# Performance work log

Hardware: AMD Instinct MI355X
Metric: run time of the kernel (lower is better)

The kernel has to match this reference:

```python
import jax, jax.numpy as jnp
import numpy as np

IN_CH = 512
MID = max(IN_CH // 8, 1)


def setup_inputs() -> dict:
    key = jax.random.key(0)
    ks = jax.random.split(key, 8)
    B, C, H, W = 4, IN_CH, 64, 64
    s = 0.05
    x = jax.random.normal(ks[0], (B, C, H, W), dtype=jnp.float32)
    wq = jax.random.normal(ks[1], (MID, C), dtype=jnp.float32) * s
    bq = jnp.zeros((MID,), dtype=jnp.float32)
    wk = jax.random.normal(ks[2], (MID, C), dtype=jnp.float32) * s
    bk = jnp.zeros((MID,), dtype=jnp.float32)
    wv = jax.random.normal(ks[3], (C, C), dtype=jnp.float32) * s
    bv = jnp.zeros((C,), dtype=jnp.float32)
    alpha = jnp.ones((1,), dtype=jnp.float32) * 0.5  # nonzero so attention path is exercised
    return {"x": x, "wq": wq, "bq": bq, "wk": wk, "bk": bk, "wv": wv, "bv": bv, "alpha": alpha}


def reference(x, wq, bq, wk, bk, wv, bv, alpha):
    B, C, H, W = x.shape
    N = H * W
    xf = x.reshape(B, C, N)  # [B, C, N]
    # 1x1 convs == per-position channel GEMMs
    q = jnp.einsum('mc,bcn->bnm', wq, xf) + bq  # [B, N, mid]
    k = jnp.einsum('mc,bcn->bmn', wk, xf) + bk[None, :, None]  # [B, mid, N]
    v = jnp.einsum('dc,bcn->bdn', wv, xf) + bv[None, :, None]  # [B, C, N]
    attn = jax.nn.softmax(jnp.einsum('bnm,bmk->bnk', q, k), axis=-1)  # [B, N, N]
    out = jnp.einsum('bdn,bkn->bdk', v, attn)  # v @ attn^T -> [B, C, N]
    out = out.reshape(B, C, H, W)
    return alpha * out + x
```

## Files before the change

kernel.cpp:

```cpp
#include <hip/hip_runtime.h>

#define BB 4
#define CD 512
#define NP 4096
#define MID 64

typedef _Float16 half8 __attribute__((ext_vector_type(8)));
typedef _Float16 half4 __attribute__((ext_vector_type(4)));
typedef float floatx4 __attribute__((ext_vector_type(4)));

#define LOG2E 1.4426950408889634f

__global__ __launch_bounds__(256) void prep_w(
    const float* __restrict__ wq, const float* __restrict__ wk,
    const float* __restrict__ wv, const float* __restrict__ bq,
    const float* __restrict__ bk, const float* __restrict__ bv,
    _Float16* __restrict__ w_h, float* __restrict__ bias) {
  int idx = blockIdx.x * 256 + threadIdx.x;
  for (int i = idx; i < 640 * 512; i += gridDim.x * 256) {
    int r = i >> 9, c = i & 511;
    float v = (r < 64) ? wq[(r << 9) + c] * LOG2E
            : (r < 128) ? wk[((r - 64) << 9) + c]
                        : wv[((r - 128) << 9) + c];
    w_h[i] = (_Float16)v;
  }
  if (idx < 640) {
    float v = (idx < 64) ? bq[idx] * LOG2E
            : (idx < 128) ? bk[idx - 64]
                          : bv[idx - 128];
    bias[idx] = v;
  }
}

__global__ __launch_bounds__(256) void transpose_x(const float* __restrict__ x,
                                                   _Float16* __restrict__ xt) {
  __shared__ float tile[64][65];
  int b = blockIdx.z, c0 = blockIdx.y * 64, n0 = blockIdx.x * 64;
  int t = threadIdx.x;
  const float* xb = x + (size_t)b * CD * NP;
#pragma unroll
  for (int k = 0; k < 16; k++) {
    int cl = k * 4 + (t >> 6);
    int nl = t & 63;
    tile[cl][nl] = xb[(size_t)(c0 + cl) * NP + n0 + nl];
  }
  __syncthreads();
  _Float16* xtb = xt + ((size_t)b * NP + n0) * CD + c0;
#pragma unroll
  for (int k = 0; k < 2; k++) {
    int nl = k * 32 + (t >> 3);
    int cl = (t & 7) * 8;
    half8 pk;
#pragma unroll
    for (int i = 0; i < 8; i++) pk[i] = (_Float16)tile[cl + i][nl];
    *(half8*)(xtb + (size_t)nl * CD + cl) = pk;
  }
}

__global__ __launch_bounds__(256, 2) void proj_qkv(
    const _Float16* __restrict__ w_h, const float* __restrict__ bias,
    const _Float16* __restrict__ xt, _Float16* __restrict__ q_h,
    _Float16* __restrict__ k_h, _Float16* __restrict__ v_h) {
  __shared__ _Float16 xls[64 * 512];
  int t = threadIdx.x, w = t >> 6, lane = t & 63;
  int col = lane & 15, quad = lane >> 4;
  int rbh = blockIdx.x, nb = blockIdx.y, b = blockIdx.z;
  int n0 = nb * 64;
  const _Float16* xtb = xt + ((size_t)b * NP + n0) * CD;
#pragma unroll
  for (int j = 0; j < 16; j++) {
    int u = t + j * 256;
    int row = u >> 6, un = u & 63;
    *(half8*)(xls + row * 512 + ((un ^ (row & 7)) << 3)) =
        *(const half8*)(xtb + (size_t)row * CD + un * 8);
  }
  __syncthreads();

  int rw = rbh * 320 + w * 80;
  floatx4 acc[5][4] = {};
  for (int c = 0; c < CD; c += 32) {
    int cu = c >> 3;
    half8 a[5], bf[4];
#pragma unroll
    for (int i = 0; i < 5; i++)
      a[i] = *(const half8*)(w_h + (size_t)(rw + i * 16 + col) * CD + c + quad * 8);
#pragma unroll
    for (int j = 0; j < 4; j++) {
      int row = j * 16 + col;
      bf[j] = *(const half8*)(xls + row * 512 + (((cu + quad) ^ (row & 7)) << 3));
    }
#pragma unroll
    for (int i = 0; i < 5; i++)
#pragma unroll
      for (int j = 0; j < 4; j++)
        acc[i][j] = __builtin_amdgcn_mfma_f32_16x16x32_f16(a[i], bf[j], acc[i][j], 0, 0, 0);
  }

#pragma unroll
  for (int i = 0; i < 5; i++) {
    int r0 = rw + i * 16;
    float bi[4];
#pragma unroll
    for (int rr = 0; rr < 4; rr++) bi[rr] = bias[r0 + quad * 4 + rr];
    if (r0 < 128) {
      _Float16* dst = (r0 < 64 ? q_h + (size_t)b * NP * MID + r0
                               : k_h + (size_t)b * NP * MID + (r0 - 64));
#pragma unroll
      for (int j = 0; j < 4; j++) {
        int n = n0 + j * 16 + col;
        half4 pk;
#pragma unroll
        for (int rr = 0; rr < 4; rr++) pk[rr] = (_Float16)(acc[i][j][rr] + bi[rr]);
        *(half4*)(dst + (size_t)n * MID + quad * 4) = pk;
      }
    } else {
      int dbase = r0 - 128 + quad * 4;
#pragma unroll
      for (int j = 0; j < 4; j++) {
        int n = n0 + j * 16 + col;
#pragma unroll
        for (int rr = 0; rr < 4; rr++)
          v_h[((size_t)b * CD + dbase + rr) * NP + n] =
              (_Float16)(acc[i][j][rr] + bi[rr]);
      }
    }
  }
}

__global__ __launch_bounds__(256) void rowmax(const _Float16* __restrict__ q_h,
                                              const _Float16* __restrict__ k_h,
                                              float* __restrict__ M) {
  int qb = blockIdx.x, b = blockIdx.y;
  int t = threadIdx.x, w = t >> 6, lane = t & 63;
  int col = lane & 15, quad = lane >> 4;
  int q0 = qb * 32;
  const _Float16* qp = q_h + ((size_t)b * NP + q0) * MID;
  half8 bq[2][2];
#pragma unroll
  for (int qt = 0; qt < 2; qt++)
#pragma unroll
    for (int h = 0; h < 2; h++)
      bq[qt][h] = *(const half8*)(qp + (size_t)(qt * 16 + col) * MID + h * 32 + quad * 8);
  const _Float16* kp = k_h + ((size_t)b * NP + (size_t)w * 1024) * MID;
  float m[2] = {-1e30f, -1e30f};
#pragma unroll 4
  for (int n = 0; n < 1024; n += 16) {
    half8 ak0 = *(const half8*)(kp + (size_t)(n + col) * MID + quad * 8);
    half8 ak1 = *(const half8*)(kp + (size_t)(n + col) * MID + 32 + quad * 8);
#pragma unroll
    for (int qt = 0; qt < 2; qt++) {
      floatx4 s = {};
      s = __builtin_amdgcn_mfma_f32_16x16x32_f16(ak0, bq[qt][0], s, 0, 0, 0);
      s = __builtin_amdgcn_mfma_f32_16x16x32_f16(ak1, bq[qt][1], s, 0, 0, 0);
      m[qt] = fmaxf(m[qt], fmaxf(fmaxf(s[0], s[1]), fmaxf(s[2], s[3])));
    }
  }
  __shared__ float red[4][2][16];
#pragma unroll
  for (int qt = 0; qt < 2; qt++) {
    m[qt] = fmaxf(m[qt], __shfl_xor(m[qt], 16));
    m[qt] = fmaxf(m[qt], __shfl_xor(m[qt], 32));
  }
  if (quad == 0) {
    red[w][0][col] = m[0];
    red[w][1][col] = m[1];
  }
  __syncthreads();
  if (t < 32) {
    int qt = t >> 4, c = t & 15;
    float mm = fmaxf(fmaxf(red[0][qt][c], red[1][qt][c]),
                     fmaxf(red[2][qt][c], red[3][qt][c]));
    M[(size_t)b * NP + q0 + t] = mm;
  }
}

#define DMA16(gp, ldsoff)                                                      \
  asm volatile("s_mov_b32 m0, %0\n\t"                                         \
               "global_load_lds_dwordx4 %1, off"                              \
               :: "s"(__builtin_amdgcn_readfirstlane((int)(ldsoff))),          \
                  "v"(gp)                                                      \
               : "memory")

__global__ __launch_bounds__(256, 2) void attn_pv(
    const _Float16* __restrict__ q_h, const _Float16* __restrict__ k_h,
    const _Float16* __restrict__ v_h, const float* __restrict__ M,
    const float* __restrict__ x, const float* __restrict__ alpha_p,
    float* __restrict__ out) {
  int bid = blockIdx.x;
  int combo = bid & 7;
  int b = combo >> 1, ds = combo & 1;
  int qb = bid >> 3;
  int q0 = qb * 64, d0 = ds * 256;

  int t = threadIdx.x, w = t >> 6, lane = t & 63;
  int col = lane & 15, quad = lane >> 4;
  int c7 = col & 7;

  __shared__ floatx4 smem4[50432 / 16];
  char* smem = (char*)smem4;
  char* vbufB = smem;
  char* kbufB = smem + 32768;
  float* lred = (float*)(smem + 49152);
  float* lfin = (float*)(smem + 50176);

  const _Float16* qp = q_h + ((size_t)b * NP + q0) * MID;
  half8 bq[4][2];
#pragma unroll
  for (int qt = 0; qt < 4; qt++)
#pragma unroll
    for (int h = 0; h < 2; h++)
      bq[qt][h] = *(const half8*)(qp + (size_t)(qt * 16 + col) * MID + h * 32 + quad * 8);
  float Mq[4];
#pragma unroll
  for (int qt = 0; qt < 4; qt++) Mq[qt] = M[(size_t)b * NP + q0 + qt * 16 + col];

  int klane = (lane >> 3) * MID + (((lane & 7) ^ ((lane >> 3) & 7)) << 3);
  size_t vlane = (size_t)(lane >> 2) * NP + ((lane & 3) << 3);

  const _Float16* kgb = k_h + (size_t)b * NP * MID;
  const _Float16* vgb = v_h + (size_t)(b * CD + d0 + w * 64) * NP;

  floatx4 acc[4][4] = {};
  float lp[4] = {0.f, 0.f, 0.f, 0.f};

  int kdw = 32768 + w * 2048;
  int vdw = w * 4096;

#pragma unroll
  for (int j = 0; j < 2; j++)
    DMA16(kgb + (size_t)(0 + w * 16 + j * 8) * MID + klane, kdw + j * 1024);
#pragma unroll
  for (int h = 0; h < 2; h++)
#pragma unroll
    for (int j = 0; j < 4; j++)
      DMA16(vgb + (size_t)(j * 16) * NP + h * 32 + vlane,
            h * 16384 + vdw + j * 1024);

  for (int ci = 0; ci < 64; ci++) {
    int p = ci & 1;
    int nxt = ((ci + 1) & 63) * 64;

    asm volatile("s_waitcnt lgkmcnt(0)\n\ts_barrier" ::: "memory");
#pragma unroll
    for (int j = 0; j < 2; j++)
      DMA16(kgb + (size_t)(nxt + w * 16 + j * 8) * MID + klane,
            kdw + (1 - p) * 8192 + j * 1024);

    asm volatile("s_waitcnt vmcnt(10)" ::: "memory");

    const char* kb = kbufB + p * 8192 + w * 2048;
    int sl0 = quad ^ c7;
    half8 ak0 = *(const half8*)(kb + col * 128 + (sl0 << 4));
    half8 ak1 = *(const half8*)(kb + col * 128 + ((sl0 ^ 4) << 4));
    char* pbW = kbufB + p * 8192;
#pragma unroll
    for (int qt = 0; qt < 4; qt++) {
      floatx4 s = {};
      s = __builtin_amdgcn_mfma_f32_16x16x32_f16(ak0, bq[qt][0], s, 0, 0, 0);
      s = __builtin_amdgcn_mfma_f32_16x16x32_f16(ak1, bq[qt][1], s, 0, 0, 0);
      half4 pk;
#pragma unroll
      for (int r = 0; r < 4; r++) {
        float pv = __builtin_amdgcn_exp2f(s[r] - Mq[qt]);
        lp[qt] += pv;
        pk[r] = (_Float16)pv;
      }
      *(half4*)(pbW + w * 2048 + (qt * 16 + col) * 32 + quad * 8) = pk;
    }

    asm volatile("s_waitcnt lgkmcnt(0)\n\ts_barrier" ::: "memory");

#pragma unroll
    for (int h = 0; h < 2; h++) {
      asm volatile("s_waitcnt vmcnt(6)" ::: "memory");
      half8 bp[4];
#pragma unroll
      for (int qt = 0; qt < 4; qt++)
        bp[qt] = *(const half8*)(pbW + (2 * h + (quad >> 1)) * 2048 +
                                 (qt * 16 + col) * 32 + ((quad & 1) << 4));
      const char* vb = vbufB + h * 16384 + vdw;
      half8 av[4];
#pragma unroll
      for (int dt = 0; dt < 4; dt++)
        av[dt] = *(const half8*)(vb + (dt * 16 + col) * 64 + (quad << 4));
      __builtin_amdgcn_s_setprio(1);
#pragma unroll
      for (int dt = 0; dt < 4; dt++)
#pragma unroll
        for (int qt = 0; qt < 4; qt++)
          acc[dt][qt] = __builtin_amdgcn_mfma_f32_16x16x32_f16(av[dt], bp[qt], acc[dt][qt], 0, 0, 0);
      __builtin_amdgcn_s_setprio(0);
#pragma unroll
      for (int j = 0; j < 4; j++)
        DMA16(vgb + (size_t)(j * 16) * NP + nxt + h * 32 + vlane,
              h * 16384 + vdw + j * 1024);
    }
  }

#pragma unroll
  for (int qt = 0; qt < 4; qt++) {
    lp[qt] += __shfl_xor(lp[qt], 16);
    lp[qt] += __shfl_xor(lp[qt], 32);
    if (quad == 0) lred[(w * 4 + qt) * 16 + col] = lp[qt];
  }
  __syncthreads();
  if (t < 64) {
    int qt = t >> 4, c = t & 15;
    float l = lred[(0 + qt) * 16 + c] + lred[(4 + qt) * 16 + c] +
              lred[(8 + qt) * 16 + c] + lred[(12 + qt) * 16 + c];
    lfin[t] = alpha_p[0] / l;
  }
  __syncthreads();

  const float* xp = x + ((size_t)(b * CD + d0) + w * 64) * NP;
  float* op = out + ((size_t)(b * CD + d0) + w * 64) * NP;
#pragma unroll
  for (int dt = 0; dt < 4; dt++)
#pragma unroll
    for (int qt = 0; qt < 4; qt++) {
      float linv = lfin[qt * 16 + col];
#pragma unroll
      for (int r = 0; r < 4; r++) {
        size_t o = (size_t)(dt * 16 + quad * 4 + r) * NP + q0 + qt * 16 + col;
        op[o] = acc[dt][qt][r] * linv + xp[o];
      }
    }
}

extern "C" void kernel_launch(void* const* d_in, const int* in_sizes, int n_in,
                              void* d_out, int out_size, void* d_ws, size_t ws_size,
                              hipStream_t stream) {
  const float* x     = (const float*)d_in[0];
  const float* wq    = (const float*)d_in[1];
  const float* bq    = (const float*)d_in[2];
  const float* wk    = (const float*)d_in[3];
  const float* bk    = (const float*)d_in[4];
  const float* wv    = (const float*)d_in[5];
  const float* bv    = (const float*)d_in[6];
  const float* alpha = (const float*)d_in[7];
  float* out = (float*)d_out;

  char* ws = (char*)d_ws;
  _Float16* w_h  = (_Float16*)(ws);
  float*    bias = (float*)(ws + 655360);
  float*    Mbuf = (float*)(ws + 657920);
  _Float16* xt   = (_Float16*)(ws + 723456);
  _Float16* q_h  = (_Float16*)(ws + 17500672);
  _Float16* k_h  = (_Float16*)(ws + 19597824);
  _Float16* v_h  = (_Float16*)(ws + 21694976);

  prep_w<<<1280, 256, 0, stream>>>(wq, wk, wv, bq, bk, bv, w_h, bias);
  transpose_x<<<dim3(64, 8, BB), 256, 0, stream>>>(x, xt);
  proj_qkv<<<dim3(2, 64, BB), 256, 0, stream>>>(w_h, bias, xt, q_h, k_h, v_h);
  rowmax<<<dim3(128, BB), 256, 0, stream>>>(q_h, k_h, Mbuf);
  attn_pv<<<512, 256, 0, stream>>>(q_h, k_h, v_h, Mbuf, x, alpha, out);
}
```

Baseline: 254.8 us.

## Software-pipeline QK/softmax one chunk ahead of PV with separate P buffer

Restructures the attention main loop so the QK scores and exp for chunk ci are computed while the PV MFMAs consume the P tile from chunk ci-1. P moves into its own double-buffered LDS region, and K becomes single-buffered. This cuts the loop to one barrier per iteration and lets the PV matrix ops overlap the softmax work. It also adds XOR swizzles to the V and P LDS layouts to reduce bank conflicts. In exchange LDS use grows, register pressure rises from holding two halves of operands, and all global loads are drained with vmcnt(0) each iteration.

```diff
diff --git a/kernel.cpp b/kernel.cpp
--- a/kernel.cpp
+++ b/kernel.cpp
@@ -196,12 +196,13 @@
   int col = lane & 15, quad = lane >> 4;
   int c7 = col & 7;
 
-  __shared__ floatx4 smem4[50432 / 16];
+  __shared__ floatx4 smem4[58624 / 16];
   char* smem = (char*)smem4;
   char* vbufB = smem;
   char* kbufB = smem + 32768;
-  float* lred = (float*)(smem + 49152);
-  float* lfin = (float*)(smem + 50176);
+  char* pbufB = smem + 40960;
+  float* lred = (float*)(smem + 57344);
+  float* lfin = (float*)(smem + 58368);
 
   const _Float16* qp = q_h + ((size_t)b * NP + q0) * MID;
   half8 bq[4][2];
@@ -215,7 +216,7 @@
   for (int qt = 0; qt < 4; qt++) Mq[qt] = M[(size_t)b * NP + q0 + qt * 16 + col];
 
   int klane = (lane >> 3) * MID + (((lane & 7) ^ ((lane >> 3) & 7)) << 3);
-  size_t vlane = (size_t)(lane >> 2) * NP + ((lane & 3) << 3);
+  size_t vlane = (size_t)(lane >> 2) * NP + (((lane & 3) ^ ((lane >> 3) & 3)) << 3);
 
   const _Float16* kgb = k_h + (size_t)b * NP * MID;
   const _Float16* vgb = v_h + (size_t)(b * CD + d0 + w * 64) * NP;
@@ -226,9 +227,15 @@
   int kdw = 32768 + w * 2048;
   int vdw = w * 4096;
 
+  int koff0 = col * 128 + ((quad ^ c7) << 4);
+  int koff1 = col * 128 + (((quad ^ c7) ^ 4) << 4);
+  int vswz = (quad ^ ((col >> 1) & 3)) << 4;
+  int pws = ((((quad >> 1) ^ ((col >> 2) & 1)) << 4)) + ((quad & 1) << 3);
+  int prs = (((quad & 1) ^ ((col >> 2) & 1)) << 4);
+
 #pragma unroll
   for (int j = 0; j < 2; j++)
-    DMA16(kgb + (size_t)(0 + w * 16 + j * 8) * MID + klane, kdw + j * 1024);
+    DMA16(kgb + (size_t)(w * 16 + j * 8) * MID + klane, kdw + j * 1024);
 #pragma unroll
   for (int h = 0; h < 2; h++)
 #pragma unroll
@@ -236,23 +243,12 @@
       DMA16(vgb + (size_t)(j * 16) * NP + h * 32 + vlane,
             h * 16384 + vdw + j * 1024);
 
-  for (int ci = 0; ci < 64; ci++) {
-    int p = ci & 1;
-    int nxt = ((ci + 1) & 63) * 64;
-
-    asm volatile("s_waitcnt lgkmcnt(0)\n\ts_barrier" ::: "memory");
-#pragma unroll
-    for (int j = 0; j < 2; j++)
-      DMA16(kgb + (size_t)(nxt + w * 16 + j * 8) * MID + klane,
-            kdw + (1 - p) * 8192 + j * 1024);
-
-    asm volatile("s_waitcnt vmcnt(10)" ::: "memory");
-
-    const char* kb = kbufB + p * 8192 + w * 2048;
-    int sl0 = quad ^ c7;
-    half8 ak0 = *(const half8*)(kb + col * 128 + (sl0 << 4));
-    half8 ak1 = *(const half8*)(kb + col * 128 + ((sl0 ^ 4) << 4));
-    char* pbW = kbufB + p * 8192;
+  asm volatile("s_waitcnt vmcnt(8)" ::: "memory");
+  {
+    const char* kb = kbufB + w * 2048;
+    half8 ak0 = *(const half8*)(kb + koff0);
+    half8 ak1 = *(const half8*)(kb + koff1);
+    char* pbW = pbufB + w * 2048;
 #pragma unroll
     for (int qt = 0; qt < 4; qt++) {
       floatx4 s = {};
@@ -265,36 +261,113 @@
         lp[qt] += pv;
         pk[r] = (_Float16)pv;
       }
-      *(half4*)(pbW + w * 2048 + (qt * 16 + col) * 32 + quad * 8) = pk;
-    }
+      *(half4*)(pbW + (qt * 16 + col) * 32 + pws) = pk;
+    }
+    asm volatile("s_waitcnt lgkmcnt(0)" ::: "memory");
+#pragma unroll
+    for (int j = 0; j < 2; j++)
+      DMA16(kgb + (size_t)(64 + w * 16 + j * 8) * MID + klane, kdw + j * 1024);
+    asm volatile("s_barrier" ::: "memory");
+  }
+
+  for (int ci = 1; ci < 64; ci++) {
+    int p = ci & 1;
+    int nc = ci * 64;
+    int nxt = ((ci + 1) & 63) * 64;
+
+    asm volatile("s_waitcnt vmcnt(0)" ::: "memory");
+
+    const char* kb = kbufB + w * 2048;
+    half8 ak0 = *(const half8*)(kb + koff0);
+    half8 ak1 = *(const half8*)(kb + koff1);
+    const char* pbR = pbufB + (1 - p) * 8192;
+    half8 bp[2][4];
+#pragma unroll
+    for (int h = 0; h < 2; h++)
+#pragma unroll
+      for (int qt = 0; qt < 4; qt++)
+        bp[h][qt] = *(const half8*)(pbR + (2 * h + (quad >> 1)) * 2048 +
+                                    (qt * 16 + col) * 32 + prs);
+    half8 av[2][4];
+#pragma unroll
+    for (int h = 0; h < 2; h++)
+#pragma unroll
+      for (int dt = 0; dt < 4; dt++)
+        av[h][dt] = *(const half8*)(vbufB + h * 16384 + vdw + dt * 1024 +
+                                    col * 64 + vswz);
+
+    floatx4 s[4];
+#pragma unroll
+    for (int qt = 0; qt < 4; qt++) {
+      floatx4 z = {};
+      z = __builtin_amdgcn_mfma_f32_16x16x32_f16(ak0, bq[qt][0], z, 0, 0, 0);
+      z = __builtin_amdgcn_mfma_f32_16x16x32_f16(ak1, bq[qt][1], z, 0, 0, 0);
+      s[qt] = z;
+    }
+
+    char* pbW = pbufB + p * 8192 + w * 2048;
+#pragma unroll
+    for (int qt = 0; qt < 4; qt++) {
+      half4 pk;
+#pragma unroll
+      for (int r = 0; r < 4; r++) {
+        float pv = __builtin_amdgcn_exp2f(s[qt][r] - Mq[qt]);
+        lp[qt] += pv;
+        pk[r] = (_Float16)pv;
+      }
+      *(half4*)(pbW + (qt * 16 + col) * 32 + pws) = pk;
+    }
+
+    asm volatile("s_waitcnt lgkmcnt(0)" ::: "memory");
+#pragma unroll
+    for (int j = 0; j < 2; j++)
+      DMA16(kgb + (size_t)(nxt + w * 16 + j * 8) * MID + klane, kdw + j * 1024);
+#pragma unroll
+    for (int h = 0; h < 2; h++)
+#pragma unroll
+      for (int j = 0; j < 4; j++)
+        DMA16(vgb + (size_t)(j * 16) * NP + nc + h * 32 + vlane,
+              h * 16384 + vdw + j * 1024);
+
+    __builtin_amdgcn_s_setprio(1);
+#pragma unroll
+    for (int h = 0; h < 2; h++)
+#pragma unroll
+      for (int dt = 0; dt < 4; dt++)
+#pragma unroll
+        for (int qt = 0; qt < 4; qt++)
+          acc[dt][qt] = __builtin_amdgcn_mfma_f32_16x16x32_f16(
+              av[h][dt], bp[h][qt], acc[dt][qt], 0, 0, 0);
+    __builtin_amdgcn_s_setprio(0);
 
     asm volatile("s_waitcnt lgkmcnt(0)\n\ts_barrier" ::: "memory");
-
-#pragma unroll
-    for (int h = 0; h < 2; h++) {
-      asm volatile("s_waitcnt vmcnt(6)" ::: "memory");
-      half8 bp[4];
+  }
+
+  asm volatile("s_waitcnt vmcnt(0)" ::: "memory");
+  {
+    const char* pbR = pbufB + 8192;
+    half8 bp[2][4];
+#pragma unroll
+    for (int h = 0; h < 2; h++)
 #pragma unroll
       for (int qt = 0; qt < 4; qt++)
-        bp[qt] = *(const half8*)(pbW + (2 * h + (quad >> 1)) * 2048 +
-                                 (qt * 16 + col) * 32 + ((quad & 1) << 4));
-      const char* vb = vbufB + h * 16384 + vdw;
-      half8 av[4];
+        bp[h][qt] = *(const half8*)(pbR + (2 * h + (quad >> 1)) * 2048 +
+                                    (qt * 16 + col) * 32 + prs);
+    half8 av[2][4];
+#pragma unroll
+    for (int h = 0; h < 2; h++)
 #pragma unroll
       for (int dt = 0; dt < 4; dt++)
-        av[dt] = *(const half8*)(vb + (dt * 16 + col) * 64 + (quad << 4));
-      __builtin_amdgcn_s_setprio(1);
+        av[h][dt] = *(const half8*)(vbufB + h * 16384 + vdw + dt * 1024 +
+                                    col * 64 + vswz);
+#pragma unroll
+    for (int h = 0; h < 2; h++)
 #pragma unroll
       for (int dt = 0; dt < 4; dt++)
 #pragma unroll
         for (int qt = 0; qt < 4; qt++)
-          acc[dt][qt] = __builtin_amdgcn_mfma_f32_16x16x32_f16(av[dt], bp[qt], acc[dt][qt], 0, 0, 0);
-      __builtin_amdgcn_s_setprio(0);
-#pragma unroll
-      for (int j = 0; j < 4; j++)
-        DMA16(vgb + (size_t)(j * 16) * NP + nxt + h * 32 + vlane,
-              h * 16384 + vdw + j * 1024);
-    }
+          acc[dt][qt] = __builtin_amdgcn_mfma_f32_16x16x32_f16(
+              av[h][dt], bp[h][qt], acc[dt][qt], 0, 0, 0);
   }
 
 #pragma unroll
```

New measurement: 255.3 us. Within noise of the previous version (+0.2%).
